# Kernel optimization log

Measured on AMD Instinct MI355X. Metric: run time of the kernel, lower is better.

Reference implementation:

```python
import jax, jax.numpy as jnp
import numpy as np

N_NODES = 100000
N_EDGES = 1600000
MSG_DIM = 16
HID_DIM = 16
N_ETYPE = 16
N_CLASSES = 64


def setup_inputs() -> dict:
    key = jax.random.key(0)
    ks = jax.random.split(key, 11)
    s = 1.0 / np.sqrt(HID_DIM)
    return {
        "features": jax.random.normal(ks[0], (N_NODES, HID_DIM), dtype=jnp.float32),
        "src": jax.random.randint(ks[1], (N_EDGES,), 0, N_NODES, dtype=jnp.int32),
        "dst": jax.random.randint(ks[2], (N_EDGES,), 0, N_NODES, dtype=jnp.int32),
        "e_type": jax.random.randint(ks[3], (N_EDGES,), 0, N_ETYPE, dtype=jnp.int32),
        "edge_emb": jax.random.normal(ks[4], (N_ETYPE, MSG_DIM * HID_DIM), dtype=jnp.float32),
        "W_ih": jax.random.uniform(ks[5], (3 * HID_DIM, MSG_DIM), dtype=jnp.float32, minval=-s, maxval=s),
        "W_hh": jax.random.uniform(ks[6], (3 * HID_DIM, HID_DIM), dtype=jnp.float32, minval=-s, maxval=s),
        "b_ih": jax.random.uniform(ks[7], (3 * HID_DIM,), dtype=jnp.float32, minval=-s, maxval=s),
        "b_hh": jax.random.uniform(ks[8], (3 * HID_DIM,), dtype=jnp.float32, minval=-s, maxval=s),
        "W_out": jax.random.normal(ks[9], (N_CLASSES, HID_DIM), dtype=jnp.float32) * s,
        "b_out": jax.random.normal(ks[10], (N_CLASSES,), dtype=jnp.float32) * 0.01,
    }


def reference(features, src, dst, e_type, edge_emb, W_ih, W_hh, b_ih, b_hh, W_out, b_out):
    # Per-edge message: A_e @ h_src, A_e = edge-type embedding reshaped [msg, hid]
    A = edge_emb[e_type].reshape(-1, MSG_DIM, HID_DIM)          # [E, M, H]
    msg = jnp.einsum("emh,eh->em", A, features[src])            # [E, M]
    # Sum-aggregate messages into destination nodes
    m = jax.ops.segment_sum(msg, dst, num_segments=N_NODES)     # [N, M]
    # Single-step GRU (PyTorch gate order: r, z, n)
    gx = m @ W_ih.T + b_ih                                      # [N, 3H]
    gh = features @ W_hh.T + b_hh                               # [N, 3H]
    xr, xz, xn = jnp.split(gx, 3, axis=-1)
    hr, hz, hn = jnp.split(gh, 3, axis=-1)
    r = jax.nn.sigmoid(xr + hr)
    z = jax.nn.sigmoid(xz + hz)
    n = jnp.tanh(xn + r * hn)
    h = (1.0 - z) * n + z * features                            # [N, H]
    return h @ W_out.T + b_out                                  # [N, C]
```

## Files before the change

kernel.cpp:

```cpp
#include <hip/hip_runtime.h>

#define NNODES 100000
#define NEDGES 1600000
#define HID 16
#define MSG 16
#define NTYPE 16
#define NCLS 64

#define BSH 7
#define NBK ((NNODES + 127) >> 7)
#define CHSZ 8192
#define NCH ((NEDGES + CHSZ - 1) / CHSZ)
#define BCAP 2304
#define BLKPB (BCAP / 256)
#define AGG_BLOCKS (NBK * BLKPB)

#define ASTR 20
#define ATY  320

__device__ __forceinline__ float sigmoid_f(float x) {
    return 1.0f / (1.0f + __expf(-x));
}
__device__ __forceinline__ float tanh_f(float x) {
    x = fminf(fmaxf(x, -15.0f), 15.0f);
    float e = __expf(2.0f * x);
    return (e - 1.0f) / (e + 1.0f);
}

__global__ __launch_bounds__(1024) void scat_k(const int* __restrict__ src,
                                               const int* __restrict__ dst,
                                               const int* __restrict__ et,
                                               int* __restrict__ gcnt,
                                               int* __restrict__ rec) {
    __shared__ int cnt[NBK];
    const int t = threadIdx.x, ch = blockIdx.x;
    for (int k = t; k < NBK; k += 1024) cnt[k] = 0;
    __syncthreads();
    int dcache[CHSZ / 1024];
    #pragma unroll
    for (int k = 0; k < CHSZ / 1024; k++) {
        int e = ch * CHSZ + k * 1024 + t;
        dcache[k] = (e < NEDGES) ? dst[e] : -1;
        if (dcache[k] >= 0) atomicAdd(&cnt[dcache[k] >> BSH], 1);
    }
    __syncthreads();
    for (int k = t; k < NBK; k += 1024) {
        int c = cnt[k];
        cnt[k] = c ? atomicAdd(&gcnt[k], c) : 0;
    }
    __syncthreads();
    #pragma unroll
    for (int k = 0; k < CHSZ / 1024; k++) {
        int e = ch * CHSZ + k * 1024 + t;
        if (e < NEDGES) {
            int d = dcache[k];
            int b = d >> BSH;
            int pos = atomicAdd(&cnt[b], 1);
            rec[b * BCAP + pos] = src[e] | (et[e] << 17) | ((d & 127) << 21);
        }
    }
}

__global__ __launch_bounds__(256) void sort2_k(const int* __restrict__ gcnt,
                                               int* __restrict__ rec) {
    __shared__ int buf[BCAP];
    __shared__ int cnt[128];
    __shared__ int basec[128];
    __shared__ int wtot[4];
    const int t = threadIdx.x, b = blockIdx.x;
    const int jb = b * BCAP;
    const int len = gcnt[b];
    if (len <= 0) return;

    if (t < 128) cnt[t] = 0;
    for (int k = t; k < len; k += 256) buf[k] = rec[jb + k];
    __syncthreads();
    for (int k = t; k < len; k += 256) atomicAdd(&cnt[((unsigned)buf[k]) >> 21], 1);
    __syncthreads();
    int v = (t < 128) ? cnt[t] : 0;
    int lane = t & 63, w = t >> 6;
    int s = v;
    #pragma unroll
    for (int d = 1; d < 64; d <<= 1) {
        int u = __shfl_up(s, d, 64);
        if (lane >= d) s += u;
    }
    if (lane == 63) wtot[w] = s;
    __syncthreads();
    if (t < 128) basec[t] = s - v + (w == 1 ? wtot[0] : 0);
    __syncthreads();
    for (int k = t; k < len; k += 256) {
        int r = buf[k];
        int p = atomicAdd(&basec[((unsigned)r) >> 21], 1);
        rec[jb + p] = r;
    }
}

__global__ __launch_bounds__(256) void agg3_k(const float* __restrict__ feat,
                                              const int* __restrict__ rec,
                                              const int* __restrict__ gcnt,
                                              const float* __restrict__ edge_emb,
                                              float* __restrict__ magg) {
    __shared__ float At2[NTYPE * ATY];
    __shared__ int recs[256];
    const int t = threadIdx.x;
    #pragma unroll
    for (int idx = t; idx < NTYPE * MSG * HID; idx += 256) {
        int ty = idx >> 8, rem = idx & 255, ii = rem >> 4, h = rem & 15;
        At2[ty * ATY + ii * ASTR + h] = edge_emb[idx];
    }
    const int b  = blockIdx.x / BLKPB;
    const int br = blockIdx.x % BLKPB;
    recs[t] = rec[b * BCAP + br * 256 + t];
    const int cnt = gcnt[b];
    __syncthreads();

    const int g = t >> 4, i = t & 15;
    const int w0 = br * 256 + (g << 4);
    int rem = cnt - w0;
    if (rem <= 0) return;
    const int vcnt = rem < 16 ? rem : 16;
    const int lbase = g << 4;

    float macc = 0.0f;
    int cur = -1;
    #pragma unroll 1
    for (int p = 0; p < 16; p += 2) {
        if (p >= vcnt) break;
        const bool has2 = (p + 1) < vcnt;
        int r1 = recs[lbase + p];
        int r2 = has2 ? recs[lbase + p + 1] : r1;
        const float4* f1 = (const float4*)(feat + (size_t)(r1 & 0x1FFFF) * HID);
        const float4* f2 = (const float4*)(feat + (size_t)(r2 & 0x1FFFF) * HID);
        float4 Fa0 = f1[0], Fa1 = f1[1], Fa2 = f1[2], Fa3 = f1[3];
        float4 Fb0 = f2[0], Fb1 = f2[1], Fb2 = f2[2], Fb3 = f2[3];
        __builtin_amdgcn_sched_barrier(0);

        {
            const float4* pa = (const float4*)(At2 + ((r1 >> 17) & 15) * ATY + i * ASTR);
            float4 A0 = pa[0], A1 = pa[1], A2 = pa[2], A3 = pa[3];
            float m1;
            m1  = A0.x*Fa0.x + A0.y*Fa0.y + A0.z*Fa0.z + A0.w*Fa0.w;
            m1 += A1.x*Fa1.x + A1.y*Fa1.y + A1.z*Fa1.z + A1.w*Fa1.w;
            m1 += A2.x*Fa2.x + A2.y*Fa2.y + A2.z*Fa2.z + A2.w*Fa2.w;
            m1 += A3.x*Fa3.x + A3.y*Fa3.y + A3.z*Fa3.z + A3.w*Fa3.w;
            int d1 = (b << BSH) | (((unsigned)r1) >> 21);
            if (d1 != cur) {
                if (cur >= 0) atomicAdd(&magg[(size_t)cur * MSG + i], macc);
                macc = 0.0f; cur = d1;
            }
            macc += m1;
        }
        if (has2) {
            const float4* pb = (const float4*)(At2 + ((r2 >> 17) & 15) * ATY + i * ASTR);
            float4 B0 = pb[0], B1 = pb[1], B2 = pb[2], B3 = pb[3];
            float m2;
            m2  = B0.x*Fb0.x + B0.y*Fb0.y + B0.z*Fb0.z + B0.w*Fb0.w;
            m2 += B1.x*Fb1.x + B1.y*Fb1.y + B1.z*Fb1.z + B1.w*Fb1.w;
            m2 += B2.x*Fb2.x + B2.y*Fb2.y + B2.z*Fb2.z + B2.w*Fb2.w;
            m2 += B3.x*Fb3.x + B3.y*Fb3.y + B3.z*Fb3.z + B3.w*Fb3.w;
            int d2 = (b << BSH) | (((unsigned)r2) >> 21);
            if (d2 != cur) {
                atomicAdd(&magg[(size_t)cur * MSG + i], macc);
                macc = 0.0f; cur = d2;
            }
            macc += m2;
        }
    }
    atomicAdd(&magg[(size_t)cur * MSG + i], macc);
}

__global__ __launch_bounds__(256) void ggnn_edge(
    const float* __restrict__ feat,
    const int* __restrict__ src,
    const int* __restrict__ dst,
    const int* __restrict__ etype,
    const float* __restrict__ edge_emb,
    float* __restrict__ magg)
{
    __shared__ float At[NTYPE * MSG * HID];
    for (int idx = threadIdx.x; idx < NTYPE * MSG * HID; idx += 256) {
        int ty = idx >> 8, rem = idx & 255, i = rem >> 4, hh = rem & 15;
        At[(ty << 8) | (hh << 4) | i] = edge_emb[idx];
    }
    __syncthreads();
    const long long total = (long long)NEDGES * MSG;
    for (long long w = (long long)blockIdx.x * 256 + threadIdx.x; w < total;
         w += (long long)gridDim.x * 256) {
        const int e = (int)(w >> 4);
        const int i = (int)(w & 15);
        const int s = src[e];
        const int d = dst[e];
        const int ty = etype[e];
        const float4* fp = (const float4*)(feat + (size_t)s * HID);
        const float4 f0 = fp[0], f1 = fp[1], f2 = fp[2], f3 = fp[3];
        const float* a = At + (ty << 8) + i;
        float m;
        m  = a[0*16]*f0.x + a[1*16]*f0.y + a[2*16]*f0.z + a[3*16]*f0.w;
        m += a[4*16]*f1.x + a[5*16]*f1.y + a[6*16]*f1.z + a[7*16]*f1.w;
        m += a[8*16]*f2.x + a[9*16]*f2.y + a[10*16]*f2.z + a[11*16]*f2.w;
        m += a[12*16]*f3.x + a[13*16]*f3.y + a[14*16]*f3.z + a[15*16]*f3.w;
        atomicAdd(magg + (size_t)d * MSG + i, m);
    }
}

__global__ __launch_bounds__(256) void node_k(
    const float* __restrict__ feat,
    const float* __restrict__ magg,
    const float* __restrict__ W_ih,
    const float* __restrict__ W_hh,
    const float* __restrict__ b_ih,
    const float* __restrict__ b_hh,
    const float* __restrict__ W_out,
    const float* __restrict__ b_out,
    float* __restrict__ out)
{
    __shared__ float hn_s[256 * 20];
    const int t = threadIdx.x;
    const int n = blockIdx.x * 256 + t;
    if (n < NNODES) {
        float hv[HID], mv[MSG];
        const float4* hp = (const float4*)(feat + (size_t)n * HID);
        const float4* mp = (const float4*)(magg + (size_t)n * MSG);
        #pragma unroll
        for (int q = 0; q < 4; q++) {
            float4 a = hp[q];
            hv[4*q+0] = a.x; hv[4*q+1] = a.y; hv[4*q+2] = a.z; hv[4*q+3] = a.w;
            float4 c = mp[q];
            mv[4*q+0] = c.x; mv[4*q+1] = c.y; mv[4*q+2] = c.z; mv[4*q+3] = c.w;
        }
        #pragma unroll
        for (int i = 0; i < HID; i++) {
            float xr = b_ih[i], xz = b_ih[16 + i], xn = b_ih[32 + i];
            float hr = b_hh[i], hz = b_hh[16 + i], hn = b_hh[32 + i];
            #pragma unroll
            for (int j = 0; j < HID; j++) {
                xr += W_ih[(i)      * 16 + j] * mv[j];
                xz += W_ih[(16 + i) * 16 + j] * mv[j];
                xn += W_ih[(32 + i) * 16 + j] * mv[j];
                hr += W_hh[(i)      * 16 + j] * hv[j];
                hz += W_hh[(16 + i) * 16 + j] * hv[j];
                hn += W_hh[(32 + i) * 16 + j] * hv[j];
            }
            float r  = sigmoid_f(xr + hr);
            float z  = sigmoid_f(xz + hz);
            float nn = tanh_f(xn + r * hn);
            hn_s[t * 20 + i] = (1.0f - z) * nn + z * hv[i];
        }
    }
    __syncthreads();

    const int w = t >> 6, g = (t >> 4) & 3, li = t & 15;
    float4 w4[4][4];
    #pragma unroll
    for (int rr = 0; rr < 4; rr++)
        #pragma unroll
        for (int qq = 0; qq < 4; qq++)
            w4[rr][qq] = ((const float4*)W_out)[(4 * li + rr) * 4 + qq];
    const float4 bo4 = ((const float4*)b_out)[li];
    const int nb = blockIdx.x * 256;

    #pragma unroll
    for (int it = 0; it < 16; it++) {
        int ln = it * 16 + w * 4 + g;
        int n2 = nb + ln;
        if (n2 < NNODES) {
            const float4* hq = (const float4*)(hn_s + ln * 20);
            float4 h0 = hq[0], h1 = hq[1], h2 = hq[2], h3 = hq[3];
            float4 o;
            o.x = bo4.x + w4[0][0].x*h0.x + w4[0][0].y*h0.y + w4[0][0].z*h0.z + w4[0][0].w*h0.w
                        + w4[0][1].x*h1.x + w4[0][1].y*h1.y + w4[0][1].z*h1.z + w4[0][1].w*h1.w
                        + w4[0][2].x*h2.x + w4[0][2].y*h2.y + w4[0][2].z*h2.z + w4[0][2].w*h2.w
                        + w4[0][3].x*h3.x + w4[0][3].y*h3.y + w4[0][3].z*h3.z + w4[0][3].w*h3.w;
            o.y = bo4.y + w4[1][0].x*h0.x + w4[1][0].y*h0.y + w4[1][0].z*h0.z + w4[1][0].w*h0.w
                        + w4[1][1].x*h1.x + w4[1][1].y*h1.y + w4[1][1].z*h1.z + w4[1][1].w*h1.w
                        + w4[1][2].x*h2.x + w4[1][2].y*h2.y + w4[1][2].z*h2.z + w4[1][2].w*h2.w
                        + w4[1][3].x*h3.x + w4[1][3].y*h3.y + w4[1][3].z*h3.z + w4[1][3].w*h3.w;
            o.z = bo4.z + w4[2][0].x*h0.x + w4[2][0].y*h0.y + w4[2][0].z*h0.z + w4[2][0].w*h0.w
                        + w4[2][1].x*h1.x + w4[2][1].y*h1.y + w4[2][1].z*h1.z + w4[2][1].w*h1.w
                        + w4[2][2].x*h2.x + w4[2][2].y*h2.y + w4[2][2].z*h2.z + w4[2][2].w*h2.w
                        + w4[2][3].x*h3.x + w4[2][3].y*h3.y + w4[2][3].z*h3.z + w4[2][3].w*h3.w;
            o.w = bo4.w + w4[3][0].x*h0.x + w4[3][0].y*h0.y + w4[3][0].z*h0.z + w4[3][0].w*h0.w
                        + w4[3][1].x*h1.x + w4[3][1].y*h1.y + w4[3][1].z*h1.z + w4[3][1].w*h1.w
                        + w4[3][2].x*h2.x + w4[3][2].y*h2.y + w4[3][2].z*h2.z + w4[3][2].w*h2.w
                        + w4[3][3].x*h3.x + w4[3][3].y*h3.y + w4[3][3].z*h3.z + w4[3][3].w*h3.w;
            ((float4*)(out + (size_t)n2 * NCLS))[li] = o;
        }
    }
}

extern "C" void kernel_launch(void* const* d_in, const int* in_sizes, int n_in,
                              void* d_out, int out_size, void* d_ws, size_t ws_size,
                              hipStream_t stream) {
    const float* feat     = (const float*)d_in[0];
    const int*   src      = (const int*)d_in[1];
    const int*   dst      = (const int*)d_in[2];
    const int*   etype    = (const int*)d_in[3];
    const float* edge_emb = (const float*)d_in[4];
    const float* W_ih     = (const float*)d_in[5];
    const float* W_hh     = (const float*)d_in[6];
    const float* b_ih     = (const float*)d_in[7];
    const float* b_hh     = (const float*)d_in[8];
    const float* W_out    = (const float*)d_in[9];
    const float* b_out    = (const float*)d_in[10];
    float* out = (float*)d_out;

    float* magg = (float*)d_ws;
    int*   gcnt = (int*)d_ws + (size_t)NNODES * MSG;
    int*   rec  = gcnt + 1024;
    size_t need = ((size_t)NNODES * MSG + 1024 + (size_t)NBK * BCAP) * 4;

    if (ws_size >= need) {
        hipMemsetAsync(magg, 0, ((size_t)NNODES * MSG + 1024) * sizeof(float), stream);
        scat_k  <<<NCH, 1024, 0, stream>>>(src, dst, etype, gcnt, rec);
        sort2_k <<<NBK, 256, 0, stream>>>(gcnt, rec);
        agg3_k  <<<AGG_BLOCKS, 256, 0, stream>>>(feat, rec, gcnt, edge_emb, magg);
    } else {
        hipMemsetAsync(magg, 0, (size_t)NNODES * MSG * sizeof(float), stream);
        ggnn_edge<<<2560, 256, 0, stream>>>(feat, src, dst, etype, edge_emb, magg);
    }
    node_k<<<(NNODES + 255) / 256, 256, 0, stream>>>(
        feat, magg, W_ih, W_hh, b_ih, b_hh, W_out, b_out, out);
}
```

Measured before the change: 136.9 us.

## Sort bucket records by edge type and accumulate per-bucket in shared memory

The in-bucket sort now keys on edge type (16 bins, serial scan) instead of destination (128 bins). The aggregation kernel uses 1024-thread blocks, three per bucket, that accumulate messages into a shared 128x17 tile with shared atomics and then flush it to global memory with one atomic per element. This drops the run-length merging of consecutive destinations, which now matters less, and aims to cut global atomic traffic and make edge-embedding reads more uniform within a wavefront. The cost is more shared-memory atomics, a full-tile flush even for sparse buckets, and a sort that now returns early when a bucket exceeds capacity.

New measurement: 242.7 us. +77.2%, slower.

```diff
diff --git a/kernel.cpp b/kernel.cpp
--- a/kernel.cpp
+++ b/kernel.cpp
@@ -12,7 +12,7 @@
 #define CHSZ 8192
 #define NCH ((NEDGES + CHSZ - 1) / CHSZ)
 #define BCAP 2304
-#define BLKPB (BCAP / 256)
+#define BLKPB 3
 #define AGG_BLOCKS (NBK * BLKPB)
 
 #define ASTR 20
@@ -64,72 +64,69 @@
 __global__ __launch_bounds__(256) void sort2_k(const int* __restrict__ gcnt,
                                                int* __restrict__ rec) {
     __shared__ int buf[BCAP];
-    __shared__ int cnt[128];
-    __shared__ int basec[128];
-    __shared__ int wtot[4];
+    __shared__ int cnt16[NTYPE];
+    __shared__ int base16[NTYPE];
     const int t = threadIdx.x, b = blockIdx.x;
     const int jb = b * BCAP;
     const int len = gcnt[b];
-    if (len <= 0) return;
-
-    if (t < 128) cnt[t] = 0;
+    if (len <= 0 || len > BCAP) return;
+
+    if (t < NTYPE) cnt16[t] = 0;
     for (int k = t; k < len; k += 256) buf[k] = rec[jb + k];
     __syncthreads();
-    for (int k = t; k < len; k += 256) atomicAdd(&cnt[((unsigned)buf[k]) >> 21], 1);
-    __syncthreads();
-    int v = (t < 128) ? cnt[t] : 0;
-    int lane = t & 63, w = t >> 6;
-    int s = v;
-    #pragma unroll
-    for (int d = 1; d < 64; d <<= 1) {
-        int u = __shfl_up(s, d, 64);
-        if (lane >= d) s += u;
-    }
-    if (lane == 63) wtot[w] = s;
-    __syncthreads();
-    if (t < 128) basec[t] = s - v + (w == 1 ? wtot[0] : 0);
+    for (int k = t; k < len; k += 256) atomicAdd(&cnt16[(buf[k] >> 17) & 15], 1);
+    __syncthreads();
+    if (t == 0) {
+        int run = 0;
+        #pragma unroll
+        for (int q = 0; q < NTYPE; q++) { base16[q] = run; run += cnt16[q]; }
+    }
     __syncthreads();
     for (int k = t; k < len; k += 256) {
         int r = buf[k];
-        int p = atomicAdd(&basec[((unsigned)r) >> 21], 1);
+        int p = atomicAdd(&base16[(r >> 17) & 15], 1);
         rec[jb + p] = r;
     }
 }
 
-__global__ __launch_bounds__(256) void agg3_k(const float* __restrict__ feat,
-                                              const int* __restrict__ rec,
-                                              const int* __restrict__ gcnt,
-                                              const float* __restrict__ edge_emb,
-                                              float* __restrict__ magg) {
+__global__ __launch_bounds__(1024, 8) void agg4_k(const float* __restrict__ feat,
+                                                  const int* __restrict__ rec,
+                                                  const int* __restrict__ gcnt,
+                                                  const float* __restrict__ edge_emb,
+                                                  float* __restrict__ magg) {
     __shared__ float At2[NTYPE * ATY];
-    __shared__ int recs[256];
+    __shared__ float acc[128 * 17];
+    __shared__ int recs[1024];
     const int t = threadIdx.x;
-    #pragma unroll
-    for (int idx = t; idx < NTYPE * MSG * HID; idx += 256) {
+    const int b  = blockIdx.x / BLKPB;
+    const int br = blockIdx.x % BLKPB;
+    const int cnt = gcnt[b];
+    const int w0 = br << 10;
+    if (w0 >= cnt) return;
+
+    #pragma unroll
+    for (int idx = t; idx < NTYPE * MSG * HID; idx += 1024) {
         int ty = idx >> 8, rem = idx & 255, ii = rem >> 4, h = rem & 15;
         At2[ty * ATY + ii * ASTR + h] = edge_emb[idx];
     }
-    const int b  = blockIdx.x / BLKPB;
-    const int br = blockIdx.x % BLKPB;
-    recs[t] = rec[b * BCAP + br * 256 + t];
-    const int cnt = gcnt[b];
-    __syncthreads();
-
-    const int g = t >> 4, i = t & 15;
-    const int w0 = br * 256 + (g << 4);
-    int rem = cnt - w0;
-    if (rem <= 0) return;
-    const int vcnt = rem < 16 ? rem : 16;
-    const int lbase = g << 4;
-
-    float macc = 0.0f;
-    int cur = -1;
+    for (int k = t; k < 128 * 17; k += 1024) acc[k] = 0.0f;
+    {
+        int ns = BCAP - w0; ns = ns > 1024 ? 1024 : ns;
+        if (t < ns) recs[t] = rec[b * BCAP + w0 + t];
+    }
+    __syncthreads();
+
+    const int G = t >> 4, i = t & 15;
+    const int base = G << 4;
+    int vr = cnt - (w0 + base);
+    const int vcnt = vr < 0 ? 0 : (vr > 16 ? 16 : vr);
+
     #pragma unroll 1
     for (int p = 0; p < 16; p += 2) {
         if (p >= vcnt) break;
-        const bool has2 = (p + 1) < vcnt;
-        int r1 = recs[lbase + p];
-        int r2 = has2 ? recs[lbase + p + 1] : r1;
+        const bool h2 = (p + 1) < vcnt;
+        int r1 = recs[base + p];
+        int r2 = h2 ? recs[base + p + 1] : r1;
         const float4* f1 = (const float4*)(feat + (size_t)(r1 & 0x1FFFF) * HID);
         const float4* f2 = (const float4*)(feat + (size_t)(r2 & 0x1FFFF) * HID);
         float4 Fa0 = f1[0], Fa1 = f1[1], Fa2 = f1[2], Fa3 = f1[3];
@@ -144,14 +141,9 @@
             m1 += A1.x*Fa1.x + A1.y*Fa1.y + A1.z*Fa1.z + A1.w*Fa1.w;
             m1 += A2.x*Fa2.x + A2.y*Fa2.y + A2.z*Fa2.z + A2.w*Fa2.w;
             m1 += A3.x*Fa3.x + A3.y*Fa3.y + A3.z*Fa3.z + A3.w*Fa3.w;
-            int d1 = (b << BSH) | (((unsigned)r1) >> 21);
-            if (d1 != cur) {
-                if (cur >= 0) atomicAdd(&magg[(size_t)cur * MSG + i], macc);
-                macc = 0.0f; cur = d1;
-            }
-            macc += m1;
-        }
-        if (has2) {
+            atomicAdd(&acc[(((unsigned)r1) >> 21) * 17 + i], m1);
+        }
+        if (h2) {
             const float4* pb = (const float4*)(At2 + ((r2 >> 17) & 15) * ATY + i * ASTR);
             float4 B0 = pb[0], B1 = pb[1], B2 = pb[2], B3 = pb[3];
             float m2;
@@ -159,15 +151,17 @@
             m2 += B1.x*Fb1.x + B1.y*Fb1.y + B1.z*Fb1.z + B1.w*Fb1.w;
             m2 += B2.x*Fb2.x + B2.y*Fb2.y + B2.z*Fb2.z + B2.w*Fb2.w;
             m2 += B3.x*Fb3.x + B3.y*Fb3.y + B3.z*Fb3.z + B3.w*Fb3.w;
-            int d2 = (b << BSH) | (((unsigned)r2) >> 21);
-            if (d2 != cur) {
-                atomicAdd(&magg[(size_t)cur * MSG + i], macc);
-                macc = 0.0f; cur = d2;
-            }
-            macc += m2;
-        }
-    }
-    atomicAdd(&magg[(size_t)cur * MSG + i], macc);
+            atomicAdd(&acc[(((unsigned)r2) >> 21) * 17 + i], m2);
+        }
+    }
+    __syncthreads();
+
+    const int nb = b << BSH;
+    for (int k = t; k < 128 * 16; k += 1024) {
+        int ln = k >> 4, ii = k & 15;
+        int n = nb + ln;
+        if (n < NNODES) atomicAdd(&magg[(size_t)n * MSG + ii], acc[ln * 17 + ii]);
+    }
 }
 
 __global__ __launch_bounds__(256) void ggnn_edge(
@@ -314,7 +308,7 @@
         hipMemsetAsync(magg, 0, ((size_t)NNODES * MSG + 1024) * sizeof(float), stream);
         scat_k  <<<NCH, 1024, 0, stream>>>(src, dst, etype, gcnt, rec);
         sort2_k <<<NBK, 256, 0, stream>>>(gcnt, rec);
-        agg3_k  <<<AGG_BLOCKS, 256, 0, stream>>>(feat, rec, gcnt, edge_emb, magg);
+        agg4_k  <<<AGG_BLOCKS, 1024, 0, stream>>>(feat, rec, gcnt, edge_emb, magg);
     } else {
         hipMemsetAsync(magg, 0, (size_t)NNODES * MSG * sizeof(float), stream);
         ggnn_edge<<<2560, 256, 0, stream>>>(feat, src, dst, etype, edge_emb, magg);
```
